# Optimization experiments

Hardware: AMD Instinct MI355X
Metric: run time of the kernel (lower is better)

Reference implementation:

```python
import jax, jax.numpy as jnp
import numpy as np

B, T, C = 4, 2048, 1024
H, D, CS = 16, 64, 16   # heads, head dim, titans chunk size
EPS = 1e-5


def setup_inputs():
    key = jax.random.key(0)
    ks = jax.random.split(key, 4)
    s = 0.02
    return {
        "x": jax.random.normal(ks[0], (B, T, C), jnp.float32),
        "W_attn": jax.random.normal(ks[1], (C, 3 * C), jnp.float32) * s,
        "b_attn": jnp.zeros((3 * C,), jnp.float32),
        "W_param": jax.random.normal(ks[2], (C, 3 * H), jnp.float32) * s,
        "b_param": jnp.zeros((3 * H,), jnp.float32),
        "W_proj": jax.random.normal(ks[3], (C, C), jnp.float32) * s,
        "b_proj": jnp.zeros((C,), jnp.float32),
        "w": jnp.ones((H, D), jnp.float32),
        "b": jnp.zeros((H, D), jnp.float32),
    }


def _ln(x, w, b):
    # per-head layernorm over last dim
    mu = x.mean(-1, keepdims=True)
    xc = x - mu
    rstd = jax.lax.rsqrt((xc * xc).mean(-1, keepdims=True) + EPS)
    return xc * rstd * w + b


def _ln_bwd(x, w, dy):
    # gradient of layernorm(x; w, b) w.r.t. x, given upstream dy
    mu = x.mean(-1, keepdims=True)
    xc = x - mu
    rstd = jax.lax.rsqrt((xc * xc).mean(-1, keepdims=True) + EPS)
    xhat = xc * rstd
    wdy = dy * w
    c1 = (xhat * wdy).mean(-1, keepdims=True)
    c2 = wdy.mean(-1, keepdims=True)
    return (wdy - xhat * c1 - c2) * rstd


def _chunk_titans_linear(q, k, v, w, b, theta, alpha, eta):
    # q,k,v: [B,H,T,D]; theta/alpha/eta: [B,H,T,1]; w,b: [H,D]
    NT = T // CS
    wr = w.reshape(1, H, 1, D)
    br = b.reshape(1, H, 1, D)

    def to_chunks(t):
        return t.reshape(B, H, NT, CS, t.shape[-1]).transpose(2, 0, 1, 3, 4)

    qc, kc, vc = to_chunks(q), to_chunks(k), to_chunks(v)
    tc, ac, ec = to_chunks(theta), to_chunks(alpha), to_chunks(eta)

    def chunk_step(carry, inp):
        S, m = carry  # memory state / momentum: [B,H,D,D]
        q_i, k_i, v_i, th_i, al_i, et_i = inp
        # gradients of ||LN(k S) - v||^2 w.r.t. S, taken at the chunk-start state
        kh = jnp.einsum('bhcd,bhde->bhce', k_i, S)
        d_recon = 2.0 * (_ln(kh, wr, br) - v_i)
        dkh = _ln_bwd(kh, wr, d_recon)
        grads = jnp.einsum('bhci,bhcj->bhcij', k_i, dkh)  # [B,H,CS,D,D]

        def tok_step(c2, t_inp):
            S_t, m_t = c2
            g, th, al, et = t_inp
            th = th[..., None]; al = al[..., None]; et = et[..., None]
            m_t = et * m_t - th * g          # momentum
            S_t = (1.0 - al) * S_t + m_t     # weight-decayed state update
            return (S_t, m_t), S_t

        (S, m), S_seq = jax.lax.scan(
            tok_step, (S, m),
            (grads.transpose(2, 0, 1, 3, 4),
             th_i.transpose(2, 0, 1, 3),
             al_i.transpose(2, 0, 1, 3),
             et_i.transpose(2, 0, 1, 3)))
        # read memory with the freshly updated per-token state
        o_i = jnp.einsum('bhcd,cbhde->bhce', q_i, S_seq)
        return (S, m), o_i

    S0 = jnp.zeros((B, H, D, D), q.dtype)
    m0 = jnp.zeros((B, H, D, D), q.dtype)
    _, o_chunks = jax.lax.scan(chunk_step, (S0, m0), (qc, kc, vc, tc, ac, ec))
    o = o_chunks.transpose(1, 2, 0, 3, 4).reshape(B, H, T, D)
    return _ln(o, wr, br)  # normalized memory readout


def reference(x, W_attn, b_attn, W_param, b_param, W_proj, b_proj, w, b):
    qkv = x @ W_attn + b_attn
    q, k, v = jnp.split(qkv, 3, axis=-1)

    def heads(t):
        return t.reshape(B, T, H, D).transpose(0, 2, 1, 3)

    q, k, v = heads(q), heads(k), heads(v)
    q = q / jnp.maximum(jnp.linalg.norm(q, axis=-1, keepdims=True), 1e-12)
    k = k / jnp.maximum(jnp.linalg.norm(k, axis=-1, keepdims=True), 1e-12)
    p = jax.nn.sigmoid((x @ W_param + b_param).reshape(B, T, H, 3).transpose(0, 2, 1, 3))
    theta, alpha, eta = p[..., 0:1], p[..., 1:2], p[..., 2:3]
    o = _chunk_titans_linear(q, k, v, w, b, theta, alpha, eta)
    o = o.transpose(0, 2, 1, 3).reshape(B, T, C)
    return o @ W_proj + b_proj
```

## Files before the change

### kernel.cpp

```cpp
#include <hip/hip_runtime.h>
#include <cstddef>
#include <cstdint>
#include <math.h>

#define BB   4
#define TT   2048
#define CCH  1024
#define HH   16
#define DD   64
#define CSZ  16
#define NTC  128
#define EPSF 1e-5f
#define WVS  8

typedef __attribute__((ext_vector_type(8))) short bf16x8;
typedef __attribute__((ext_vector_type(4))) float f32x4;

__device__ __forceinline__ uint32_t pack_split(float f) {
  uint32_t b = __float_as_uint(f);
  uint32_t uh = (b + 0x7fffu + ((b >> 16) & 1u)) >> 16;
  float fh = __uint_as_float(uh << 16);
  float r = f - fh;
  return uh | (__float_as_uint(r) & 0xffff0000u);
}
__device__ __forceinline__ float unpack_f(uint32_t u) {
  return __uint_as_float(u << 16) + __uint_as_float(u & 0xffff0000u);
}

__device__ __forceinline__ float wave_sum(float x) {
  float v = x;
  v += __int_as_float(__builtin_amdgcn_update_dpp(0, __float_as_int(v), 0x111, 0xf, 0xf, true));
  v += __int_as_float(__builtin_amdgcn_update_dpp(0, __float_as_int(v), 0x112, 0xf, 0xf, true));
  v += __int_as_float(__builtin_amdgcn_update_dpp(0, __float_as_int(v), 0x114, 0xf, 0xf, true));
  v += __int_as_float(__builtin_amdgcn_update_dpp(0, __float_as_int(v), 0x118, 0xf, 0xf, true));
  v += __int_as_float(__builtin_amdgcn_update_dpp(0, __float_as_int(v), 0x142, 0xa, 0xf, true));
  v += __int_as_float(__builtin_amdgcn_update_dpp(0, __float_as_int(v), 0x143, 0xc, 0xf, true));
  return __int_as_float(__builtin_amdgcn_readlane(__float_as_int(v), 63));
}

__device__ __forceinline__ float sigmoidf_(float x) {
  return 1.f / (1.f + expf(-x));
}

__global__ __launch_bounds__(256) void split_transpose(
    const float* __restrict__ W, uint32_t* __restrict__ Wt, int K, int N) {
  __shared__ float t[32][33];
  const int n0 = blockIdx.x * 32, k0 = blockIdx.y * 32;
  const int tx = threadIdx.x & 31, ty = threadIdx.x >> 5;
#pragma unroll
  for (int i = 0; i < 4; i++)
    t[ty + i * 8][tx] = W[(size_t)(k0 + ty + i * 8) * N + n0 + tx];
  __syncthreads();
#pragma unroll
  for (int i = 0; i < 4; i++)
    Wt[(size_t)(n0 + ty + i * 8) * K + k0 + tx] = pack_split(t[tx][ty + i * 8]);
}

template<bool A_PACKED, bool C_PACKED>
__global__ __launch_bounds__(256) void gemm_split(
    const void* __restrict__ Av, int lda,
    const uint32_t* __restrict__ Bt,
    const float* __restrict__ bias,
    void* __restrict__ Cv, int M, int N, int K) {
  __shared__ unsigned short Ahi[128][40];
  __shared__ unsigned short Alo[128][40];
  __shared__ unsigned short Bhi[128][40];
  __shared__ unsigned short Blo[128][40];

  const int tid = threadIdx.x;
  const int row0 = blockIdx.y * 128;
  const int col0 = blockIdx.x * 128;
  const int wv = tid >> 6;
  const int l  = tid & 63;
  const int wr = wv >> 1, wc = wv & 1;
  const int lrow = l & 15;
  const int kgrp = (l >> 4) * 8;

  const int sr = tid >> 1;
  const int sk = (tid & 1) * 16;

  f32x4 acc[4][4];
#pragma unroll
  for (int i = 0; i < 4; i++)
#pragma unroll
    for (int j = 0; j < 4; j++) acc[i][j] = (f32x4){0.f, 0.f, 0.f, 0.f};

  for (int k0 = 0; k0 < K; k0 += 32) {
    {
      uint32_t hp[8], lp[8];
      if (A_PACKED) {
        const uint32_t* Ap = (const uint32_t*)Av + (size_t)(row0 + sr) * lda + k0 + sk;
        uint32_t u[16];
#pragma unroll
        for (int i = 0; i < 4; i++) *(uint4*)&u[i * 4] = *(const uint4*)(Ap + i * 4);
#pragma unroll
        for (int j = 0; j < 8; j++) {
          hp[j] = (u[2 * j] & 0xffffu) | (u[2 * j + 1] << 16);
          lp[j] = (u[2 * j] >> 16) | (u[2 * j + 1] & 0xffff0000u);
        }
      } else {
        const float* Ap = (const float*)Av + (size_t)(row0 + sr) * lda + k0 + sk;
        float f[16];
#pragma unroll
        for (int i = 0; i < 4; i++) *(float4*)&f[i * 4] = *(const float4*)(Ap + i * 4);
        uint32_t uh[16], ulr[16];
#pragma unroll
        for (int j = 0; j < 16; j++) {
          uint32_t b = __float_as_uint(f[j]);
          uint32_t h = (b + 0x7fffu + ((b >> 16) & 1u)) >> 16;
          uh[j] = h;
          ulr[j] = __float_as_uint(f[j] - __uint_as_float(h << 16));
        }
#pragma unroll
        for (int j = 0; j < 8; j++) {
          hp[j] = uh[2 * j] | (uh[2 * j + 1] << 16);
          lp[j] = (ulr[2 * j] >> 16) | (ulr[2 * j + 1] & 0xffff0000u);
        }
      }
      *(uint4*)&Ahi[sr][sk]     = *(uint4*)&hp[0];
      *(uint4*)&Ahi[sr][sk + 8] = *(uint4*)&hp[4];
      *(uint4*)&Alo[sr][sk]     = *(uint4*)&lp[0];
      *(uint4*)&Alo[sr][sk + 8] = *(uint4*)&lp[4];
    }
    {
      const uint32_t* Bp = Bt + (size_t)(col0 + sr) * K + k0 + sk;
      uint32_t u[16], hp[8], lp[8];
#pragma unroll
      for (int i = 0; i < 4; i++) *(uint4*)&u[i * 4] = *(const uint4*)(Bp + i * 4);
#pragma unroll
      for (int j = 0; j < 8; j++) {
        hp[j] = (u[2 * j] & 0xffffu) | (u[2 * j + 1] << 16);
        lp[j] = (u[2 * j] >> 16) | (u[2 * j + 1] & 0xffff0000u);
      }
      *(uint4*)&Bhi[sr][sk]     = *(uint4*)&hp[0];
      *(uint4*)&Bhi[sr][sk + 8] = *(uint4*)&hp[4];
      *(uint4*)&Blo[sr][sk]     = *(uint4*)&lp[0];
      *(uint4*)&Blo[sr][sk + 8] = *(uint4*)&lp[4];
    }
    __syncthreads();

    bf16x8 bh[4], bl[4];
#pragma unroll
    for (int j = 0; j < 4; j++) {
      bh[j] = *(const bf16x8*)&Bhi[wc * 64 + j * 16 + lrow][kgrp];
      bl[j] = *(const bf16x8*)&Blo[wc * 64 + j * 16 + lrow][kgrp];
    }
#pragma unroll
    for (int i = 0; i < 4; i++) {
      bf16x8 ah = *(const bf16x8*)&Ahi[wr * 64 + i * 16 + lrow][kgrp];
      bf16x8 al = *(const bf16x8*)&Alo[wr * 64 + i * 16 + lrow][kgrp];
#pragma unroll
      for (int j = 0; j < 4; j++) {
        acc[i][j] = __builtin_amdgcn_mfma_f32_16x16x32_bf16(ah, bh[j], acc[i][j], 0, 0, 0);
        acc[i][j] = __builtin_amdgcn_mfma_f32_16x16x32_bf16(ah, bl[j], acc[i][j], 0, 0, 0);
        acc[i][j] = __builtin_amdgcn_mfma_f32_16x16x32_bf16(al, bh[j], acc[i][j], 0, 0, 0);
      }
    }
    __syncthreads();
  }

  const int crow4 = (l >> 4) * 4;
#pragma unroll
  for (int i = 0; i < 4; i++) {
#pragma unroll
    for (int j = 0; j < 4; j++) {
      const int col = col0 + wc * 64 + j * 16 + lrow;
      const float bv = bias[col];
      const int rowb = row0 + wr * 64 + i * 16 + crow4;
#pragma unroll
      for (int r = 0; r < 4; r++) {
        float v = acc[i][j][r] + bv;
        size_t off = (size_t)(rowb + r) * N + col;
        if (C_PACKED) ((uint32_t*)Cv)[off] = pack_split(v);
        else          ((float*)Cv)[off] = v;
      }
    }
  }
}

__global__ __launch_bounds__(256) void gemm_f32(
    const float* __restrict__ A, int lda,
    const float* __restrict__ W,
    const float* __restrict__ bias,
    float* __restrict__ C, int M, int N, int K) {
  __shared__ float As[16][132];
  __shared__ float Bs[16][128];
  const int tid  = threadIdx.x;
  const int row0 = blockIdx.y * 128;
  const int col0 = blockIdx.x * 128;
  const int ty = tid >> 4;
  const int tx = tid & 15;
  const int a_r = tid >> 2;
  const int a_k = (tid & 3) << 2;
  const int b_r = tid >> 5;
  const int b_c = (tid & 31) << 2;

  float acc[8][8];
#pragma unroll
  for (int i = 0; i < 8; i++)
#pragma unroll
    for (int j = 0; j < 8; j++) acc[i][j] = 0.f;

  float4 areg[2], breg[2];
  const int gc = col0 + b_c;
#pragma unroll
  for (int i = 0; i < 2; i++)
    areg[i] = *(const float4*)(A + (size_t)(row0 + a_r + i * 64) * lda + a_k);
#pragma unroll
  for (int i = 0; i < 2; i++) {
    breg[i] = make_float4(0.f, 0.f, 0.f, 0.f);
    if (gc < N) breg[i] = *(const float4*)(W + (size_t)(b_r + i * 8) * N + gc);
  }

  for (int k0 = 0; k0 < K; k0 += 16) {
#pragma unroll
    for (int i = 0; i < 2; i++) {
      int r = a_r + i * 64;
      As[a_k + 0][r] = areg[i].x;
      As[a_k + 1][r] = areg[i].y;
      As[a_k + 2][r] = areg[i].z;
      As[a_k + 3][r] = areg[i].w;
    }
#pragma unroll
    for (int i = 0; i < 2; i++) *(float4*)(&Bs[b_r + i * 8][b_c]) = breg[i];
    __syncthreads();

    if (k0 + 16 < K) {
#pragma unroll
      for (int i = 0; i < 2; i++)
        areg[i] = *(const float4*)(A + (size_t)(row0 + a_r + i * 64) * lda + (k0 + 16 + a_k));
#pragma unroll
      for (int i = 0; i < 2; i++) {
        breg[i] = make_float4(0.f, 0.f, 0.f, 0.f);
        if (gc < N) breg[i] = *(const float4*)(W + (size_t)(k0 + 16 + b_r + i * 8) * N + gc);
      }
    }

#pragma unroll
    for (int kk = 0; kk < 16; kk++) {
      float af[8], bf[8];
      *(float4*)&af[0] = *(const float4*)&As[kk][ty * 8];
      *(float4*)&af[4] = *(const float4*)&As[kk][ty * 8 + 4];
      *(float4*)&bf[0] = *(const float4*)&Bs[kk][tx * 8];
      *(float4*)&bf[4] = *(const float4*)&Bs[kk][tx * 8 + 4];
#pragma unroll
      for (int i = 0; i < 8; i++)
#pragma unroll
        for (int j = 0; j < 8; j++) acc[i][j] += af[i] * bf[j];
    }
    __syncthreads();
  }
#pragma unroll
  for (int i = 0; i < 8; i++) {
    int r = row0 + ty * 8 + i;
#pragma unroll
    for (int j0 = 0; j0 < 8; j0 += 4) {
      int cc = col0 + tx * 8 + j0;
      if (cc < N) {
        float4 ov;
        ov.x = acc[i][j0 + 0] + bias[cc + 0];
        ov.y = acc[i][j0 + 1] + bias[cc + 1];
        ov.z = acc[i][j0 + 2] + bias[cc + 2];
        ov.w = acc[i][j0 + 3] + bias[cc + 3];
        *(float4*)(C + (size_t)r * N + cc) = ov;
      }
    }
  }
}

__global__ __launch_bounds__(256) void normalize_qk(uint32_t* __restrict__ qkv) {
  const int idx = blockIdx.x * 4 + (threadIdx.x >> 6);
  const int l = threadIdx.x & 63;
  const int rowBT = idx >> 5;
  const int rem = idx & 31;
  const int which = rem >> 4;
  const int h = rem & 15;
  const size_t addr = (size_t)rowBT * 3072 + (size_t)which * 1024 + h * 64 + l;
  float v = unpack_f(qkv[addr]);
  float ss = wave_sum(v * v);
  float sc = 1.f / fmaxf(sqrtf(ss), 1e-12f);
  qkv[addr] = pack_split(v * sc);
}

__global__ __launch_bounds__(512) void titans_rec(
    uint32_t* __restrict__ qkv, const float* __restrict__ p,
    const float* __restrict__ w, const float* __restrict__ bparm) {
  const int bh = blockIdx.x;
  const int b = bh >> 4;
  const int h = bh & 15;
  const int tid = threadIdx.x;
  const int wv = tid >> 6;
  const int l = tid & 63;

  __shared__ float k_s[2][CSZ][DD];
  __shared__ float q_s[2][CSZ][DD];
  __shared__ float v_s[CSZ][DD];
  __shared__ float dkh_s[CSZ][DD];
  __shared__ float part[2][WVS][CSZ][DD];
  __shared__ float4 prm_s[2][CSZ];

  float S[8], M[8];
#pragma unroll
  for (int r = 0; r < 8; r++) { S[r] = 0.f; M[r] = 0.f; }

  const float w_l = w[h * DD + l];
  const float b_l = bparm[h * DD + l];

  uint32_t* qbase = qkv + (size_t)(b * TT) * 3072 + h * DD;
  const float* pbase = p + (size_t)(b * TT) * 48 + h * 3;

  uint32_t rq[2], rk[2], rv[2];
  float rp0 = 0.f, rp1 = 0.f, rp2 = 0.f;
  {
#pragma unroll
    for (int i = 0; i < 2; i++) {
      int row = wv + i * 8;
      size_t roff = (size_t)row * 3072 + l;
      q_s[0][row][l] = unpack_f(qbase[roff]);
      k_s[0][row][l] = unpack_f(qbase[roff + 1024]);
      v_s[row][l]    = unpack_f(qbase[roff + 2048]);
    }
    if (tid < CSZ) {
      const float* pp = pbase + (size_t)tid * 48;
      prm_s[0][tid] = make_float4(sigmoidf_(pp[0]), sigmoidf_(pp[1]), sigmoidf_(pp[2]), 0.f);
    }
#pragma unroll
    for (int i = 0; i < 2; i++) {
      size_t roff = (size_t)(CSZ + wv + i * 8) * 3072 + l;
      rq[i] = qbase[roff];
      rk[i] = qbase[roff + 1024];
      rv[i] = qbase[roff + 2048];
    }
    if (tid < CSZ) {
      const float* pp = pbase + (size_t)(CSZ + tid) * 48;
      rp0 = pp[0]; rp1 = pp[1]; rp2 = pp[2];
    }
  }
  __syncthreads();

  for (int nt = 0; nt < NTC; nt++) {
    const int buf = nt & 1;
    float (*partw)[CSZ][DD] = part[buf];
    float (*partr)[CSZ][DD] = part[buf ^ 1];

    if (nt > 0) {
#pragma unroll
      for (int i = 0; i < 2; i++) {
        const int t = wv + i * 8;
        float o = 0.f;
#pragma unroll
        for (int ww = 0; ww < WVS; ww++) o += partr[ww][t][l];
        float mu = wave_sum(o) * (1.f / 64.f);
        float xc = o - mu;
        float var = wave_sum(xc * xc) * (1.f / 64.f);
        float rstd = rsqrtf(var + EPSF);
        float y = xc * rstd * w_l + b_l;
        qbase[(size_t)((nt - 1) * CSZ + t) * 3072 + 2048 + l] = pack_split(y);
      }
    }
#pragma unroll
    for (int c = 0; c < CSZ; c++) {
      const float* kp = &k_s[buf][c][wv * 8];
      float4 ka = *(const float4*)kp;
      float4 kb = *(const float4*)(kp + 4);
      partw[wv][c][l] = ka.x * S[0] + ka.y * S[1] + ka.z * S[2] + ka.w * S[3]
                      + kb.x * S[4] + kb.y * S[5] + kb.z * S[6] + kb.w * S[7];
    }
    __syncthreads();

#pragma unroll
    for (int i = 0; i < 2; i++) {
      const int c = wv + i * 8;
      float kh = 0.f;
#pragma unroll
      for (int ww = 0; ww < WVS; ww++) kh += partw[ww][c][l];
      float mu = wave_sum(kh) * (1.f / 64.f);
      float xc = kh - mu;
      float var = wave_sum(xc * xc) * (1.f / 64.f);
      float rstd = rsqrtf(var + EPSF);
      float xhat = xc * rstd;
      float y = xhat * w_l + b_l;
      float dy = 2.f * (y - v_s[c][l]);
      float wdy = dy * w_l;
      float c1 = wave_sum(xhat * wdy) * (1.f / 64.f);
      float c2 = wave_sum(wdy) * (1.f / 64.f);
      dkh_s[c][l] = (wdy - xhat * c1 - c2) * rstd;
    }
    __syncthreads();

    if (nt + 1 < NTC) {
#pragma unroll
      for (int i = 0; i < 2; i++) {
        int row = wv + i * 8;
        k_s[buf ^ 1][row][l] = unpack_f(rk[i]);
        q_s[buf ^ 1][row][l] = unpack_f(rq[i]);
        v_s[row][l] = unpack_f(rv[i]);
      }
      if (tid < CSZ)
        prm_s[buf ^ 1][tid] = make_float4(sigmoidf_(rp0), sigmoidf_(rp1), sigmoidf_(rp2), 0.f);
    }
    if (nt + 2 < NTC) {
#pragma unroll
      for (int i = 0; i < 2; i++) {
        size_t roff = (size_t)((nt + 2) * CSZ + wv + i * 8) * 3072 + l;
        rq[i] = qbase[roff];
        rk[i] = qbase[roff + 1024];
        rv[i] = qbase[roff + 2048];
      }
      if (tid < CSZ) {
        const float* pp = pbase + (size_t)((nt + 2) * CSZ + tid) * 48;
        rp0 = pp[0]; rp1 = pp[1]; rp2 = pp[2];
      }
    }
#pragma unroll
    for (int t = 0; t < CSZ; t++) {
      float4 prm = prm_s[buf][t];
      float a = prm.x * dkh_s[t][l];
      float et = prm.z;
      float bet = 1.f - prm.y;
      const float* kp = &k_s[buf][t][wv * 8];
      const float* qp = &q_s[buf][t][wv * 8];
      float4 ka = *(const float4*)kp, kb = *(const float4*)(kp + 4);
      float4 qa = *(const float4*)qp, qb = *(const float4*)(qp + 4);
      float po;
      M[0] = et * M[0] - a * ka.x;  S[0] = bet * S[0] + M[0];  po  = qa.x * S[0];
      M[1] = et * M[1] - a * ka.y;  S[1] = bet * S[1] + M[1];  po += qa.y * S[1];
      M[2] = et * M[2] - a * ka.z;  S[2] = bet * S[2] + M[2];  po += qa.z * S[2];
      M[3] = et * M[3] - a * ka.w;  S[3] = bet * S[3] + M[3];  po += qa.w * S[3];
      M[4] = et * M[4] - a * kb.x;  S[4] = bet * S[4] + M[4];  po += qb.x * S[4];
      M[5] = et * M[5] - a * kb.y;  S[5] = bet * S[5] + M[5];  po += qb.y * S[5];
      M[6] = et * M[6] - a * kb.z;  S[6] = bet * S[6] + M[6];  po += qb.z * S[6];
      M[7] = et * M[7] - a * kb.w;  S[7] = bet * S[7] + M[7];  po += qb.w * S[7];
      partw[wv][t][l] = po;
    }
    __syncthreads();
  }

  {
    float (*partr)[CSZ][DD] = part[(NTC - 1) & 1];
#pragma unroll
    for (int i = 0; i < 2; i++) {
      const int t = wv + i * 8;
      float o = 0.f;
#pragma unroll
      for (int ww = 0; ww < WVS; ww++) o += partr[ww][t][l];
      float mu = wave_sum(o) * (1.f / 64.f);
      float xc = o - mu;
      float var = wave_sum(xc * xc) * (1.f / 64.f);
      float rstd = rsqrtf(var + EPSF);
      float y = xc * rstd * w_l + b_l;
      qbase[(size_t)((NTC - 1) * CSZ + t) * 3072 + 2048 + l] = pack_split(y);
    }
  }
}

extern "C" void kernel_launch(void* const* d_in, const int* in_sizes, int n_in,
                              void* d_out, int out_size, void* d_ws, size_t ws_size,
                              hipStream_t stream) {
  const float* x      = (const float*)d_in[0];
  const float* W_attn = (const float*)d_in[1];
  const float* b_attn = (const float*)d_in[2];
  const float* W_parm = (const float*)d_in[3];
  const float* b_parm = (const float*)d_in[4];
  const float* W_proj = (const float*)d_in[5];
  const float* b_proj = (const float*)d_in[6];
  const float* w      = (const float*)d_in[7];
  const float* bb     = (const float*)d_in[8];
  float* out = (float*)d_out;

  const int M = BB * TT;
  float* qkv = (float*)d_ws;
  float* pbf = qkv + (size_t)M * 3072;
  uint32_t* wattn_t = (uint32_t*)(pbf + (size_t)M * 48);
  uint32_t* wproj_t = wattn_t + (size_t)3072 * 1024;

  split_transpose<<<dim3(3072 / 32, 1024 / 32), 256, 0, stream>>>(W_attn, wattn_t, 1024, 3072);
  split_transpose<<<dim3(1024 / 32, 1024 / 32), 256, 0, stream>>>(W_proj, wproj_t, 1024, 1024);

  gemm_split<false, true><<<dim3(3072 / 128, M / 128), 256, 0, stream>>>(
      x, CCH, wattn_t, b_attn, qkv, M, 3072, CCH);
  gemm_f32<<<dim3(1, M / 128), 256, 0, stream>>>(x, CCH, W_parm, b_parm, pbf, M, 48, CCH);
  normalize_qk<<<(M * 2 * HH) / 4, 256, 0, stream>>>((uint32_t*)qkv);
  titans_rec<<<BB * HH, 512, 0, stream>>>((uint32_t*)qkv, pbf, w, bb);
  gemm_split<true, false><<<dim3(CCH / 128, M / 128), 256, 0, stream>>>(
      (uint32_t*)qkv + 2048, 3072, wproj_t, b_proj, out, M, CCH, CCH);
}
```

Baseline: 1.057 ms.

## Reformulate chunk recurrence in closed form and use split-bf16 MFMA for matmuls

Replaces the per-token sequential state/momentum update with a closed-form chunk formulation. It precomputes decay products (A, B, E coefficients and an intra-chunk weight matrix C∘(QKᵀ)) and computes outputs as a·(Q S) + b·(Q M) − W·dKH, using three-term split-bf16 MFMA products on transposed S/M tiles held in LDS. The end-of-chunk state update is computed directly from weighted sums over the chunk. This cuts the serial per-token dependency chain and the cross-wave partial-sum reduction. In exchange it adds extra barriers, LDS traffic for the hi/lo state copies and pack/unpack overhead, and it changes numerics slightly through the split-bf16 approximation.

```diff
diff --git a/kernel.cpp b/kernel.cpp
--- a/kernel.cpp
+++ b/kernel.cpp
@@ -11,7 +11,6 @@
 #define CSZ  16
 #define NTC  128
 #define EPSF 1e-5f
-#define WVS  8
 
 typedef __attribute__((ext_vector_type(8))) short bf16x8;
 typedef __attribute__((ext_vector_type(4))) float f32x4;
@@ -291,13 +290,23 @@
   const int tid = threadIdx.x;
   const int wv = tid >> 6;
   const int l = tid & 63;
-
-  __shared__ float k_s[2][CSZ][DD];
-  __shared__ float q_s[2][CSZ][DD];
-  __shared__ float v_s[CSZ][DD];
+  const int lr = l & 15;
+  const int kg = (l >> 4) * 8;
+
+  __shared__ unsigned short Sthi[64][72], Stlo[64][72];
+  __shared__ unsigned short Mthi[64][72], Mtlo[64][72];
+  __shared__ unsigned short Khi[16][72], Klo[16][72];
+  __shared__ unsigned short Qhi[16][72], Qlo[16][72];
+  __shared__ unsigned short DThi[64][32], DTlo[64][32];
+  __shared__ unsigned short Whi[16][32], Wlo[16][32];
+  __shared__ float k_s[CSZ][DD], v_s[CSZ][DD];
+  __shared__ float kh_s[CSZ][66], o_s[CSZ][66];
   __shared__ float dkh_s[CSZ][DD];
-  __shared__ float part[2][WVS][CSZ][DD];
-  __shared__ float4 prm_s[2][CSZ];
+  __shared__ float g_s[CSZ][CSZ];
+  __shared__ float c_s[CSZ][CSZ];
+  __shared__ float a_s[CSZ], b_s[CSZ], rvec_s[CSZ];
+  __shared__ float sc_s[4];
+  __shared__ float4 prm_s[CSZ];
 
   float S[8], M[8];
 #pragma unroll
@@ -309,71 +318,122 @@
   uint32_t* qbase = qkv + (size_t)(b * TT) * 3072 + h * DD;
   const float* pbase = p + (size_t)(b * TT) * 48 + h * 3;
 
+  for (int i = tid; i < 2304; i += 512) {
+    ((uint32_t*)Sthi)[i] = 0; ((uint32_t*)Stlo)[i] = 0;
+    ((uint32_t*)Mthi)[i] = 0; ((uint32_t*)Mtlo)[i] = 0;
+  }
+  for (int i = tid; i < 1024; i += 512) { ((uint32_t*)DThi)[i] = 0; ((uint32_t*)DTlo)[i] = 0; }
+  if (tid < 256) { ((uint32_t*)Whi)[tid] = 0; ((uint32_t*)Wlo)[tid] = 0; }
+  {
+#pragma unroll
+    for (int i = 0; i < 2; i++) {
+      const int row = wv + i * 8;
+      size_t roff = (size_t)row * 3072 + l;
+      uint32_t uq = qbase[roff], uk = qbase[roff + 1024], uv = qbase[roff + 2048];
+      k_s[row][l] = unpack_f(uk);
+      v_s[row][l] = unpack_f(uv);
+      Khi[row][l] = (unsigned short)(uk & 0xffffu); Klo[row][l] = (unsigned short)(uk >> 16);
+      Qhi[row][l] = (unsigned short)(uq & 0xffffu); Qlo[row][l] = (unsigned short)(uq >> 16);
+    }
+    if (tid < CSZ) {
+      const float* pp = pbase + (size_t)tid * 48;
+      prm_s[tid] = make_float4(sigmoidf_(pp[0]), sigmoidf_(pp[1]), sigmoidf_(pp[2]), 0.f);
+    }
+  }
+  __syncthreads();
+
   uint32_t rq[2], rk[2], rv[2];
   float rp0 = 0.f, rp1 = 0.f, rp2 = 0.f;
-  {
-#pragma unroll
-    for (int i = 0; i < 2; i++) {
-      int row = wv + i * 8;
-      size_t roff = (size_t)row * 3072 + l;
-      q_s[0][row][l] = unpack_f(qbase[roff]);
-      k_s[0][row][l] = unpack_f(qbase[roff + 1024]);
-      v_s[row][l]    = unpack_f(qbase[roff + 2048]);
-    }
-    if (tid < CSZ) {
-      const float* pp = pbase + (size_t)tid * 48;
-      prm_s[0][tid] = make_float4(sigmoidf_(pp[0]), sigmoidf_(pp[1]), sigmoidf_(pp[2]), 0.f);
-    }
-#pragma unroll
-    for (int i = 0; i < 2; i++) {
-      size_t roff = (size_t)(CSZ + wv + i * 8) * 3072 + l;
-      rq[i] = qbase[roff];
-      rk[i] = qbase[roff + 1024];
-      rv[i] = qbase[roff + 2048];
-    }
-    if (tid < CSZ) {
-      const float* pp = pbase + (size_t)(CSZ + tid) * 48;
-      rp0 = pp[0]; rp1 = pp[1]; rp2 = pp[2];
-    }
-  }
-  __syncthreads();
 
   for (int nt = 0; nt < NTC; nt++) {
-    const int buf = nt & 1;
-    float (*partw)[CSZ][DD] = part[buf];
-    float (*partr)[CSZ][DD] = part[buf ^ 1];
-
-    if (nt > 0) {
+    f32x4 accS = (f32x4){0.f, 0.f, 0.f, 0.f};
+    f32x4 accM = (f32x4){0.f, 0.f, 0.f, 0.f};
+
+    if (nt + 1 < NTC) {
 #pragma unroll
       for (int i = 0; i < 2; i++) {
-        const int t = wv + i * 8;
-        float o = 0.f;
-#pragma unroll
-        for (int ww = 0; ww < WVS; ww++) o += partr[ww][t][l];
-        float mu = wave_sum(o) * (1.f / 64.f);
-        float xc = o - mu;
-        float var = wave_sum(xc * xc) * (1.f / 64.f);
-        float rstd = rsqrtf(var + EPSF);
-        float y = xc * rstd * w_l + b_l;
-        qbase[(size_t)((nt - 1) * CSZ + t) * 3072 + 2048 + l] = pack_split(y);
-      }
-    }
-#pragma unroll
-    for (int c = 0; c < CSZ; c++) {
-      const float* kp = &k_s[buf][c][wv * 8];
-      float4 ka = *(const float4*)kp;
-      float4 kb = *(const float4*)(kp + 4);
-      partw[wv][c][l] = ka.x * S[0] + ka.y * S[1] + ka.z * S[2] + ka.w * S[3]
-                      + kb.x * S[4] + kb.y * S[5] + kb.z * S[6] + kb.w * S[7];
+        size_t roff = (size_t)((nt + 1) * CSZ + wv + i * 8) * 3072 + l;
+        rq[i] = qbase[roff]; rk[i] = qbase[roff + 1024]; rv[i] = qbase[roff + 2048];
+      }
+      if (tid < CSZ) {
+        const float* pp = pbase + (size_t)((nt + 1) * CSZ + tid) * 48;
+        rp0 = pp[0]; rp1 = pp[1]; rp2 = pp[2];
+      }
+    }
+    if (wv < 4) {
+      f32x4 acc = (f32x4){0.f, 0.f, 0.f, 0.f};
+#pragma unroll
+      for (int ks = 0; ks < 2; ks++) {
+        const int ko = kg + ks * 32;
+        bf16x8 ah = *(const bf16x8*)&Khi[lr][ko];
+        bf16x8 aL = *(const bf16x8*)&Klo[lr][ko];
+        bf16x8 bh = *(const bf16x8*)&Sthi[wv * 16 + lr][ko];
+        bf16x8 bL = *(const bf16x8*)&Stlo[wv * 16 + lr][ko];
+        acc = __builtin_amdgcn_mfma_f32_16x16x32_bf16(ah, bh, acc, 0, 0, 0);
+        acc = __builtin_amdgcn_mfma_f32_16x16x32_bf16(ah, bL, acc, 0, 0, 0);
+        acc = __builtin_amdgcn_mfma_f32_16x16x32_bf16(aL, bh, acc, 0, 0, 0);
+      }
+#pragma unroll
+      for (int r = 0; r < 4; r++) kh_s[(l >> 4) * 4 + r][wv * 16 + lr] = acc[r];
+    } else {
+      const int et = (wv - 4) * 16 + lr;
+      f32x4 accG = (f32x4){0.f, 0.f, 0.f, 0.f};
+#pragma unroll
+      for (int ks = 0; ks < 2; ks++) {
+        const int ko = kg + ks * 32;
+        bf16x8 ah = *(const bf16x8*)&Qhi[lr][ko];
+        bf16x8 aL = *(const bf16x8*)&Qlo[lr][ko];
+        bf16x8 bh = *(const bf16x8*)&Sthi[et][ko];
+        bf16x8 bL = *(const bf16x8*)&Stlo[et][ko];
+        accS = __builtin_amdgcn_mfma_f32_16x16x32_bf16(ah, bh, accS, 0, 0, 0);
+        accS = __builtin_amdgcn_mfma_f32_16x16x32_bf16(ah, bL, accS, 0, 0, 0);
+        accS = __builtin_amdgcn_mfma_f32_16x16x32_bf16(aL, bh, accS, 0, 0, 0);
+        bh = *(const bf16x8*)&Mthi[et][ko];
+        bL = *(const bf16x8*)&Mtlo[et][ko];
+        accM = __builtin_amdgcn_mfma_f32_16x16x32_bf16(ah, bh, accM, 0, 0, 0);
+        accM = __builtin_amdgcn_mfma_f32_16x16x32_bf16(ah, bL, accM, 0, 0, 0);
+        accM = __builtin_amdgcn_mfma_f32_16x16x32_bf16(aL, bh, accM, 0, 0, 0);
+        if (wv == 4) {
+          bf16x8 gh = *(const bf16x8*)&Khi[lr][ko];
+          bf16x8 gL = *(const bf16x8*)&Klo[lr][ko];
+          accG = __builtin_amdgcn_mfma_f32_16x16x32_bf16(ah, gh, accG, 0, 0, 0);
+          accG = __builtin_amdgcn_mfma_f32_16x16x32_bf16(ah, gL, accG, 0, 0, 0);
+          accG = __builtin_amdgcn_mfma_f32_16x16x32_bf16(aL, gh, accG, 0, 0, 0);
+        }
+      }
+      if (wv == 4) {
+#pragma unroll
+        for (int r = 0; r < 4; r++) g_s[(l >> 4) * 4 + r][lr] = accG[r];
+      }
+    }
+    if (wv == 5 && l < 16) {
+      float A = 1.f, Bc = 0.f, E = 1.f;
+      for (int i = 0; i <= l; i++) {
+        float4 pr = prm_s[i];
+        float bet = 1.f - pr.y;
+        E *= pr.z;
+        A *= bet;
+        Bc = bet * Bc + E;
+      }
+      a_s[l] = A; b_s[l] = Bc;
+      if (l == 15) { sc_s[0] = A; sc_s[1] = Bc; sc_s[2] = E; }
+      float th_l = prm_s[l].x;
+      float R = 1.f, D = 1.f;
+      c_s[l][l] = th_l;
+      for (int t = l + 1; t < 16; t++) {
+        float4 pr = prm_s[t];
+        R *= pr.z;
+        D = (1.f - pr.y) * D + R;
+        c_s[t][l] = th_l * D;
+      }
+      rvec_s[l] = th_l * R;
     }
     __syncthreads();
 
 #pragma unroll
     for (int i = 0; i < 2; i++) {
       const int c = wv + i * 8;
-      float kh = 0.f;
-#pragma unroll
-      for (int ww = 0; ww < WVS; ww++) kh += partw[ww][c][l];
+      float kh = kh_s[c][l];
       float mu = wave_sum(kh) * (1.f / 64.f);
       float xc = kh - mu;
       float var = wave_sum(xc * xc) * (1.f / 64.f);
@@ -386,71 +446,112 @@
       float c2 = wave_sum(wdy) * (1.f / 64.f);
       dkh_s[c][l] = (wdy - xhat * c1 - c2) * rstd;
     }
-    __syncthreads();
-
+    if (tid < 256) {
+      const int t = tid >> 4, lc = tid & 15;
+      float wval = (lc <= t) ? c_s[t][lc] * g_s[t][lc] : 0.f;
+      uint32_t ps = pack_split(wval);
+      Whi[t][lc] = (unsigned short)(ps & 0xffffu);
+      Wlo[t][lc] = (unsigned short)(ps >> 16);
+    }
+    __syncthreads();
+
+    {
+      const int idx = tid * 2;
+      const int e = idx >> 4, t = idx & 15;
+      uint32_t p0 = pack_split(dkh_s[t][e]);
+      uint32_t p1 = pack_split(dkh_s[t + 1][e]);
+      *(uint32_t*)&DThi[e][t] = (p0 & 0xffffu) | ((p1 & 0xffffu) << 16);
+      *(uint32_t*)&DTlo[e][t] = (p0 >> 16) | (p1 & 0xffff0000u);
+    }
+    __syncthreads();
+
+    if (wv >= 4) {
+      const int et = (wv - 4) * 16 + lr;
+      f32x4 accO = (f32x4){0.f, 0.f, 0.f, 0.f};
+      bf16x8 ah = *(const bf16x8*)&Whi[lr][kg];
+      bf16x8 aL = *(const bf16x8*)&Wlo[lr][kg];
+      bf16x8 bh = *(const bf16x8*)&DThi[et][kg];
+      bf16x8 bL = *(const bf16x8*)&DTlo[et][kg];
+      accO = __builtin_amdgcn_mfma_f32_16x16x32_bf16(ah, bh, accO, 0, 0, 0);
+      accO = __builtin_amdgcn_mfma_f32_16x16x32_bf16(ah, bL, accO, 0, 0, 0);
+      accO = __builtin_amdgcn_mfma_f32_16x16x32_bf16(aL, bh, accO, 0, 0, 0);
+#pragma unroll
+      for (int r = 0; r < 4; r++) {
+        const int t = (l >> 4) * 4 + r;
+        o_s[t][et] = a_s[t] * accS[r] + b_s[t] * accM[r] - accO[r];
+      }
+    }
+    {
+      const float a15 = sc_s[0], b15 = sc_s[1], e15 = sc_s[2];
+      float sS[8], sM[8];
+#pragma unroll
+      for (int r = 0; r < 8; r++) { sS[r] = 0.f; sM[r] = 0.f; }
+#pragma unroll 4
+      for (int t = 0; t < 16; t++) {
+        float dt = dkh_s[t][l];
+        float cd = c_s[15][t] * dt;
+        float rd = rvec_s[t] * dt;
+        const float* kp = &k_s[t][wv * 8];
+        float4 ka = *(const float4*)kp;
+        float4 kb = *(const float4*)(kp + 4);
+        sS[0] += cd * ka.x; sM[0] += rd * ka.x;
+        sS[1] += cd * ka.y; sM[1] += rd * ka.y;
+        sS[2] += cd * ka.z; sM[2] += rd * ka.z;
+        sS[3] += cd * ka.w; sM[3] += rd * ka.w;
+        sS[4] += cd * kb.x; sM[4] += rd * kb.x;
+        sS[5] += cd * kb.y; sM[5] += rd * kb.y;
+        sS[6] += cd * kb.z; sM[6] += rd * kb.z;
+        sS[7] += cd * kb.w; sM[7] += rd * kb.w;
+      }
+#pragma unroll
+      for (int r = 0; r < 8; r++) {
+        float So = S[r];
+        S[r] = a15 * So + b15 * M[r] - sS[r];
+        M[r] = e15 * M[r] - sM[r];
+      }
+    }
+    __syncthreads();
+
+    {
+      uint32_t ps[8], pm[8];
+#pragma unroll
+      for (int r = 0; r < 8; r++) { ps[r] = pack_split(S[r]); pm[r] = pack_split(M[r]); }
+      uint4 sh, sl, mh, ml;
+      sh.x = (ps[0] & 0xffffu) | (ps[1] << 16);  sl.x = (ps[0] >> 16) | (ps[1] & 0xffff0000u);
+      sh.y = (ps[2] & 0xffffu) | (ps[3] << 16);  sl.y = (ps[2] >> 16) | (ps[3] & 0xffff0000u);
+      sh.z = (ps[4] & 0xffffu) | (ps[5] << 16);  sl.z = (ps[4] >> 16) | (ps[5] & 0xffff0000u);
+      sh.w = (ps[6] & 0xffffu) | (ps[7] << 16);  sl.w = (ps[6] >> 16) | (ps[7] & 0xffff0000u);
+      mh.x = (pm[0] & 0xffffu) | (pm[1] << 16);  ml.x = (pm[0] >> 16) | (pm[1] & 0xffff0000u);
+      mh.y = (pm[2] & 0xffffu) | (pm[3] << 16);  ml.y = (pm[2] >> 16) | (pm[3] & 0xffff0000u);
+      mh.z = (pm[4] & 0xffffu) | (pm[5] << 16);  ml.z = (pm[4] >> 16) | (pm[5] & 0xffff0000u);
+      mh.w = (pm[6] & 0xffffu) | (pm[7] << 16);  ml.w = (pm[6] >> 16) | (pm[7] & 0xffff0000u);
+      *(uint4*)&Sthi[l][wv * 8] = sh;  *(uint4*)&Stlo[l][wv * 8] = sl;
+      *(uint4*)&Mthi[l][wv * 8] = mh;  *(uint4*)&Mtlo[l][wv * 8] = ml;
+    }
     if (nt + 1 < NTC) {
 #pragma unroll
       for (int i = 0; i < 2; i++) {
-        int row = wv + i * 8;
-        k_s[buf ^ 1][row][l] = unpack_f(rk[i]);
-        q_s[buf ^ 1][row][l] = unpack_f(rq[i]);
+        const int row = wv + i * 8;
+        k_s[row][l] = unpack_f(rk[i]);
         v_s[row][l] = unpack_f(rv[i]);
+        Khi[row][l] = (unsigned short)(rk[i] & 0xffffu); Klo[row][l] = (unsigned short)(rk[i] >> 16);
+        Qhi[row][l] = (unsigned short)(rq[i] & 0xffffu); Qlo[row][l] = (unsigned short)(rq[i] >> 16);
       }
       if (tid < CSZ)
-        prm_s[buf ^ 1][tid] = make_float4(sigmoidf_(rp0), sigmoidf_(rp1), sigmoidf_(rp2), 0.f);
-    }
-    if (nt + 2 < NTC) {
-#pragma unroll
-      for (int i = 0; i < 2; i++) {
-        size_t roff = (size_t)((nt + 2) * CSZ + wv + i * 8) * 3072 + l;
-        rq[i] = qbase[roff];
-        rk[i] = qbase[roff + 1024];
-        rv[i] = qbase[roff + 2048];
-      }
-      if (tid < CSZ) {
-        const float* pp = pbase + (size_t)((nt + 2) * CSZ + tid) * 48;
-        rp0 = pp[0]; rp1 = pp[1]; rp2 = pp[2];
-      }
-    }
-#pragma unroll
-    for (int t = 0; t < CSZ; t++) {
-      float4 prm = prm_s[buf][t];
-      float a = prm.x * dkh_s[t][l];
-      float et = prm.z;
-      float bet = 1.f - prm.y;
-      const float* kp = &k_s[buf][t][wv * 8];
-      const float* qp = &q_s[buf][t][wv * 8];
-      float4 ka = *(const float4*)kp, kb = *(const float4*)(kp + 4);
-      float4 qa = *(const float4*)qp, qb = *(const float4*)(qp + 4);
-      float po;
-      M[0] = et * M[0] - a * ka.x;  S[0] = bet * S[0] + M[0];  po  = qa.x * S[0];
-      M[1] = et * M[1] - a * ka.y;  S[1] = bet * S[1] + M[1];  po += qa.y * S[1];
-      M[2] = et * M[2] - a * ka.z;  S[2] = bet * S[2] + M[2];  po += qa.z * S[2];
-      M[3] = et * M[3] - a * ka.w;  S[3] = bet * S[3] + M[3];  po += qa.w * S[3];
-      M[4] = et * M[4] - a * kb.x;  S[4] = bet * S[4] + M[4];  po += qb.x * S[4];
-      M[5] = et * M[5] - a * kb.y;  S[5] = bet * S[5] + M[5];  po += qb.y * S[5];
-      M[6] = et * M[6] - a * kb.z;  S[6] = bet * S[6] + M[6];  po += qb.z * S[6];
-      M[7] = et * M[7] - a * kb.w;  S[7] = bet * S[7] + M[7];  po += qb.w * S[7];
-      partw[wv][t][l] = po;
-    }
-    __syncthreads();
-  }
-
-  {
-    float (*partr)[CSZ][DD] = part[(NTC - 1) & 1];
+        prm_s[tid] = make_float4(sigmoidf_(rp0), sigmoidf_(rp1), sigmoidf_(rp2), 0.f);
+    }
 #pragma unroll
     for (int i = 0; i < 2; i++) {
       const int t = wv + i * 8;
-      float o = 0.f;
-#pragma unroll
-      for (int ww = 0; ww < WVS; ww++) o += partr[ww][t][l];
+      float o = o_s[t][l];
       float mu = wave_sum(o) * (1.f / 64.f);
       float xc = o - mu;
       float var = wave_sum(xc * xc) * (1.f / 64.f);
       float rstd = rsqrtf(var + EPSF);
       float y = xc * rstd * w_l + b_l;
-      qbase[(size_t)((NTC - 1) * CSZ + t) * 3072 + 2048 + l] = pack_split(y);
-    }
+      qbase[(size_t)(nt * CSZ + t) * 3072 + 2048 + l] = pack_split(y);
+    }
+    __syncthreads();
   }
 }
 
```

New measurement: 1.187 ms. 12.3% more time.

## Fuse q/k normalization into recurrence, store weight hi/lo planes, prefetch GEMM tiles

Applied to the files above, without the earlier changes.

Removes the standalone normalize_qk pass and instead L2-normalizes q and k rows inside titans_rec as they are loaded into shared memory. This saves a full read-modify-write of the q/k portion of the qkv buffer. The pre-transposed weights are now stored as separate hi and lo bf16 planes, so the GEMM can copy B straight into LDS without unpacking. The GEMM main loop also register-prefetches the next K tile before the MFMA work to overlap global loads with compute. The recurrence kernel gains extra wave reductions on its serial critical path, which may offset part of the saved pass.

```diff
diff --git a/kernel.cpp b/kernel.cpp
--- a/kernel.cpp
+++ b/kernel.cpp
@@ -42,8 +42,9 @@
   return 1.f / (1.f + expf(-x));
 }
 
-__global__ __launch_bounds__(256) void split_transpose(
-    const float* __restrict__ W, uint32_t* __restrict__ Wt, int K, int N) {
+__global__ __launch_bounds__(256) void split_transpose_pl(
+    const float* __restrict__ W, unsigned short* __restrict__ Whi,
+    unsigned short* __restrict__ Wlo, int K, int N) {
   __shared__ float t[32][33];
   const int n0 = blockIdx.x * 32, k0 = blockIdx.y * 32;
   const int tx = threadIdx.x & 31, ty = threadIdx.x >> 5;
@@ -52,16 +53,21 @@
     t[ty + i * 8][tx] = W[(size_t)(k0 + ty + i * 8) * N + n0 + tx];
   __syncthreads();
 #pragma unroll
-  for (int i = 0; i < 4; i++)
-    Wt[(size_t)(n0 + ty + i * 8) * K + k0 + tx] = pack_split(t[tx][ty + i * 8]);
-}
-
-template<bool A_PACKED, bool C_PACKED>
-__global__ __launch_bounds__(256) void gemm_split(
+  for (int i = 0; i < 4; i++) {
+    uint32_t ps = pack_split(t[tx][ty + i * 8]);
+    size_t off = (size_t)(n0 + ty + i * 8) * K + k0 + tx;
+    Whi[off] = (unsigned short)(ps & 0xffffu);
+    Wlo[off] = (unsigned short)(ps >> 16);
+  }
+}
+
+template<int AMODE, bool C_PACKED>
+__global__ __launch_bounds__(256) void gemm_planes(
     const void* __restrict__ Av, int lda,
-    const uint32_t* __restrict__ Bt,
-    const float* __restrict__ bias,
-    void* __restrict__ Cv, int M, int N, int K) {
+    const unsigned short* __restrict__ Bhg,
+    const unsigned short* __restrict__ Blg,
+    const float* __restrict__ bias, void* __restrict__ Cv,
+    int M, int N, int K) {
   __shared__ unsigned short Ahi[128][40];
   __shared__ unsigned short Alo[128][40];
   __shared__ unsigned short Bhi[128][40];
@@ -75,7 +81,6 @@
   const int wr = wv >> 1, wc = wv & 1;
   const int lrow = l & 15;
   const int kgrp = (l >> 4) * 8;
-
   const int sr = tid >> 1;
   const int sk = (tid & 1) * 16;
 
@@ -85,59 +90,70 @@
 #pragma unroll
     for (int j = 0; j < 4; j++) acc[i][j] = (f32x4){0.f, 0.f, 0.f, 0.f};
 
-  for (int k0 = 0; k0 < K; k0 += 32) {
-    {
-      uint32_t hp[8], lp[8];
-      if (A_PACKED) {
-        const uint32_t* Ap = (const uint32_t*)Av + (size_t)(row0 + sr) * lda + k0 + sk;
-        uint32_t u[16];
-#pragma unroll
-        for (int i = 0; i < 4; i++) *(uint4*)&u[i * 4] = *(const uint4*)(Ap + i * 4);
-#pragma unroll
-        for (int j = 0; j < 8; j++) {
-          hp[j] = (u[2 * j] & 0xffffu) | (u[2 * j + 1] << 16);
-          lp[j] = (u[2 * j] >> 16) | (u[2 * j + 1] & 0xffff0000u);
-        }
-      } else {
-        const float* Ap = (const float*)Av + (size_t)(row0 + sr) * lda + k0 + sk;
-        float f[16];
-#pragma unroll
-        for (int i = 0; i < 4; i++) *(float4*)&f[i * 4] = *(const float4*)(Ap + i * 4);
-        uint32_t uh[16], ulr[16];
-#pragma unroll
-        for (int j = 0; j < 16; j++) {
-          uint32_t b = __float_as_uint(f[j]);
-          uint32_t h = (b + 0x7fffu + ((b >> 16) & 1u)) >> 16;
-          uh[j] = h;
-          ulr[j] = __float_as_uint(f[j] - __uint_as_float(h << 16));
-        }
-#pragma unroll
-        for (int j = 0; j < 8; j++) {
-          hp[j] = uh[2 * j] | (uh[2 * j + 1] << 16);
-          lp[j] = (ulr[2 * j] >> 16) | (ulr[2 * j + 1] & 0xffff0000u);
-        }
-      }
-      *(uint4*)&Ahi[sr][sk]     = *(uint4*)&hp[0];
-      *(uint4*)&Ahi[sr][sk + 8] = *(uint4*)&hp[4];
-      *(uint4*)&Alo[sr][sk]     = *(uint4*)&lp[0];
-      *(uint4*)&Alo[sr][sk + 8] = *(uint4*)&lp[4];
-    }
-    {
-      const uint32_t* Bp = Bt + (size_t)(col0 + sr) * K + k0 + sk;
-      uint32_t u[16], hp[8], lp[8];
-#pragma unroll
-      for (int i = 0; i < 4; i++) *(uint4*)&u[i * 4] = *(const uint4*)(Bp + i * 4);
+  uint4 pa[4];
+  float4 pf[4];
+  uint4 pb[4];
+
+  auto load_tile = [&](int k0) {
+    if (AMODE == 1) {
+      const uint32_t* Ap = (const uint32_t*)Av + (size_t)(row0 + sr) * lda + k0 + sk;
+#pragma unroll
+      for (int i = 0; i < 4; i++) pa[i] = *(const uint4*)(Ap + i * 4);
+    } else {
+      const float* Ap = (const float*)Av + (size_t)(row0 + sr) * lda + k0 + sk;
+#pragma unroll
+      for (int i = 0; i < 4; i++) pf[i] = *(const float4*)(Ap + i * 4);
+    }
+    const unsigned short* bh = Bhg + (size_t)(col0 + sr) * K + k0 + sk;
+    const unsigned short* bl = Blg + (size_t)(col0 + sr) * K + k0 + sk;
+    pb[0] = *(const uint4*)bh;  pb[1] = *(const uint4*)(bh + 8);
+    pb[2] = *(const uint4*)bl;  pb[3] = *(const uint4*)(bl + 8);
+  };
+
+  auto commit_tile = [&]() {
+    uint32_t hp[8], lp[8];
+    if (AMODE == 1) {
+      uint32_t u[16];
+#pragma unroll
+      for (int i = 0; i < 4; i++) *(uint4*)&u[i * 4] = pa[i];
 #pragma unroll
       for (int j = 0; j < 8; j++) {
         hp[j] = (u[2 * j] & 0xffffu) | (u[2 * j + 1] << 16);
         lp[j] = (u[2 * j] >> 16) | (u[2 * j + 1] & 0xffff0000u);
       }
-      *(uint4*)&Bhi[sr][sk]     = *(uint4*)&hp[0];
-      *(uint4*)&Bhi[sr][sk + 8] = *(uint4*)&hp[4];
-      *(uint4*)&Blo[sr][sk]     = *(uint4*)&lp[0];
-      *(uint4*)&Blo[sr][sk + 8] = *(uint4*)&lp[4];
-    }
-    __syncthreads();
+    } else {
+      float f[16];
+#pragma unroll
+      for (int i = 0; i < 4; i++) *(float4*)&f[i * 4] = pf[i];
+      uint32_t uh[16], ulr[16];
+#pragma unroll
+      for (int j = 0; j < 16; j++) {
+        uint32_t b = __float_as_uint(f[j]);
+        uint32_t h = (b + 0x7fffu + ((b >> 16) & 1u)) >> 16;
+        uh[j] = h;
+        ulr[j] = __float_as_uint(f[j] - __uint_as_float(h << 16));
+      }
+#pragma unroll
+      for (int j = 0; j < 8; j++) {
+        hp[j] = uh[2 * j] | (uh[2 * j + 1] << 16);
+        lp[j] = (ulr[2 * j] >> 16) | (ulr[2 * j + 1] & 0xffff0000u);
+      }
+    }
+    *(uint4*)&Ahi[sr][sk]     = *(uint4*)&hp[0];
+    *(uint4*)&Ahi[sr][sk + 8] = *(uint4*)&hp[4];
+    *(uint4*)&Alo[sr][sk]     = *(uint4*)&lp[0];
+    *(uint4*)&Alo[sr][sk + 8] = *(uint4*)&lp[4];
+    *(uint4*)&Bhi[sr][sk]     = pb[0];
+    *(uint4*)&Bhi[sr][sk + 8] = pb[1];
+    *(uint4*)&Blo[sr][sk]     = pb[2];
+    *(uint4*)&Blo[sr][sk + 8] = pb[3];
+  };
+
+  load_tile(0);
+  for (int k0 = 0; k0 < K; k0 += 32) {
+    commit_tile();
+    __syncthreads();
+    if (k0 + 32 < K) load_tile(k0 + 32);
 
     bf16x8 bh[4], bl[4];
 #pragma unroll
@@ -268,20 +284,6 @@
   }
 }
 
-__global__ __launch_bounds__(256) void normalize_qk(uint32_t* __restrict__ qkv) {
-  const int idx = blockIdx.x * 4 + (threadIdx.x >> 6);
-  const int l = threadIdx.x & 63;
-  const int rowBT = idx >> 5;
-  const int rem = idx & 31;
-  const int which = rem >> 4;
-  const int h = rem & 15;
-  const size_t addr = (size_t)rowBT * 3072 + (size_t)which * 1024 + h * 64 + l;
-  float v = unpack_f(qkv[addr]);
-  float ss = wave_sum(v * v);
-  float sc = 1.f / fmaxf(sqrtf(ss), 1e-12f);
-  qkv[addr] = pack_split(v * sc);
-}
-
 __global__ __launch_bounds__(512) void titans_rec(
     uint32_t* __restrict__ qkv, const float* __restrict__ p,
     const float* __restrict__ w, const float* __restrict__ bparm) {
@@ -314,11 +316,16 @@
   {
 #pragma unroll
     for (int i = 0; i < 2; i++) {
-      int row = wv + i * 8;
+      const int row = wv + i * 8;
       size_t roff = (size_t)row * 3072 + l;
-      q_s[0][row][l] = unpack_f(qbase[roff]);
-      k_s[0][row][l] = unpack_f(qbase[roff + 1024]);
-      v_s[row][l]    = unpack_f(qbase[roff + 2048]);
+      float qv = unpack_f(qbase[roff]);
+      float kv = unpack_f(qbase[roff + 1024]);
+      float vv = unpack_f(qbase[roff + 2048]);
+      float qss = wave_sum(qv * qv);
+      float kss = wave_sum(kv * kv);
+      q_s[0][row][l] = qv * (1.f / fmaxf(sqrtf(qss), 1e-12f));
+      k_s[0][row][l] = kv * (1.f / fmaxf(sqrtf(kss), 1e-12f));
+      v_s[row][l] = vv;
     }
     if (tid < CSZ) {
       const float* pp = pbase + (size_t)tid * 48;
@@ -391,9 +398,13 @@
     if (nt + 1 < NTC) {
 #pragma unroll
       for (int i = 0; i < 2; i++) {
-        int row = wv + i * 8;
-        k_s[buf ^ 1][row][l] = unpack_f(rk[i]);
-        q_s[buf ^ 1][row][l] = unpack_f(rq[i]);
+        const int row = wv + i * 8;
+        float qv = unpack_f(rq[i]);
+        float kv = unpack_f(rk[i]);
+        float qss = wave_sum(qv * qv);
+        float kss = wave_sum(kv * kv);
+        q_s[buf ^ 1][row][l] = qv * (1.f / fmaxf(sqrtf(qss), 1e-12f));
+        k_s[buf ^ 1][row][l] = kv * (1.f / fmaxf(sqrtf(kss), 1e-12f));
         v_s[row][l] = unpack_f(rv[i]);
       }
       if (tid < CSZ)
@@ -471,17 +482,18 @@
   const int M = BB * TT;
   float* qkv = (float*)d_ws;
   float* pbf = qkv + (size_t)M * 3072;
-  uint32_t* wattn_t = (uint32_t*)(pbf + (size_t)M * 48);
-  uint32_t* wproj_t = wattn_t + (size_t)3072 * 1024;
-
-  split_transpose<<<dim3(3072 / 32, 1024 / 32), 256, 0, stream>>>(W_attn, wattn_t, 1024, 3072);
-  split_transpose<<<dim3(1024 / 32, 1024 / 32), 256, 0, stream>>>(W_proj, wproj_t, 1024, 1024);
-
-  gemm_split<false, true><<<dim3(3072 / 128, M / 128), 256, 0, stream>>>(
-      x, CCH, wattn_t, b_attn, qkv, M, 3072, CCH);
+  unsigned short* wattn_hi = (unsigned short*)(pbf + (size_t)M * 48);
+  unsigned short* wattn_lo = wattn_hi + (size_t)3072 * 1024;
+  unsigned short* wproj_hi = wattn_lo + (size_t)3072 * 1024;
+  unsigned short* wproj_lo = wproj_hi + (size_t)1024 * 1024;
+
+  split_transpose_pl<<<dim3(3072 / 32, 1024 / 32), 256, 0, stream>>>(W_attn, wattn_hi, wattn_lo, 1024, 3072);
+  split_transpose_pl<<<dim3(1024 / 32, 1024 / 32), 256, 0, stream>>>(W_proj, wproj_hi, wproj_lo, 1024, 1024);
+
+  gemm_planes<2, true><<<dim3(3072 / 128, M / 128), 256, 0, stream>>>(
+      x, CCH, wattn_hi, wattn_lo, b_attn, qkv, M, 3072, CCH);
   gemm_f32<<<dim3(1, M / 128), 256, 0, stream>>>(x, CCH, W_parm, b_parm, pbf, M, 48, CCH);
-  normalize_qk<<<(M * 2 * HH) / 4, 256, 0, stream>>>((uint32_t*)qkv);
   titans_rec<<<BB * HH, 512, 0, stream>>>((uint32_t*)qkv, pbf, w, bb);
-  gemm_split<true, false><<<dim3(CCH / 128, M / 128), 256, 0, stream>>>(
-      (uint32_t*)qkv + 2048, 3072, wproj_t, b_proj, out, M, CCH, CCH);
-}
+  gemm_planes<1, false><<<dim3(CCH / 128, M / 128), 256, 0, stream>>>(
+      (uint32_t*)qkv + 2048, 3072, wproj_hi, wproj_lo, b_proj, out, M, CCH, CCH);
+}
```

Result: slower. 1.238 ms (+17.1%).
